# Optimization experiments

Measured on AMD Instinct MI355X. Metric: run time of the kernel, lower is better.

## Reference

```python
import jax, jax.numpy as jnp
import numpy as np

WEIGHT_HARD = 0.5
WEIGHT_SOFT = 0.5
BETA = 0.5
IGNORE_INDEX = -100
TEMPERATURE = 1.0

N_TOK = 2048
H_STU = 2048
H_TEA = 4096
VOCAB = 32000


def setup_inputs() -> dict:
    key = jax.random.key(0)
    k1, k2, k3, k4, k5 = jax.random.split(key, 5)
    scale_s = 1.0 / np.sqrt(H_STU)
    scale_t = 1.0 / np.sqrt(H_TEA)
    return {
        "student_input": jax.random.normal(k1, (N_TOK, H_STU), dtype=jnp.float32),
        "student_weight": jax.random.normal(k2, (VOCAB, H_STU), dtype=jnp.float32) * scale_s,
        "teacher_input": jax.random.normal(k3, (N_TOK, H_TEA), dtype=jnp.float32),
        "teacher_weight": jax.random.normal(k4, (VOCAB, H_TEA), dtype=jnp.float32) * scale_t,
        "true_labels": jax.random.randint(k5, (N_TOK,), 0, VOCAB, dtype=jnp.int64),
    }


def reference(student_input, student_weight, teacher_input, teacher_weight, true_labels):
    n = student_input.shape[0]
    # Fused linear projections: (BT, H) @ (H, V) -> (BT, V)
    s_logits = jnp.einsum("nh,vh->nv", student_input, student_weight).astype(jnp.float32)
    t_logits = jnp.einsum("nh,vh->nv", teacher_input, teacher_weight).astype(jnp.float32)

    # Hard loss: NLL on un-tempered student log-probs, sum over valid, / total N
    s_lp = jax.nn.log_softmax(s_logits, axis=-1)
    valid = true_labels != IGNORE_INDEX
    safe_labels = jnp.where(valid, true_labels, 0)
    picked = jnp.take_along_axis(s_lp, safe_labels[:, None], axis=1)[:, 0]
    hard_loss = jnp.sum(jnp.where(valid, -picked, 0.0)) / n

    # Soft loss: generalized JSD on temperature-scaled logits, sum over all tokens, / N
    s_lp_t = jax.nn.log_softmax(s_logits / TEMPERATURE, axis=-1)
    t_lp_t = jax.nn.log_softmax(t_logits / TEMPERATURE, axis=-1)
    s_p = jnp.exp(s_lp_t)
    t_p = jnp.exp(t_lp_t)
    log_mean = jnp.log(BETA * s_p + (1.0 - BETA) * t_p)
    student_kl = jnp.sum(s_p * (s_lp_t - log_mean))  # KL(student || mean)
    teacher_kl = jnp.sum(t_p * (t_lp_t - log_mean))  # KL(teacher || mean)
    jsd = BETA * teacher_kl + (1.0 - BETA) * student_kl
    soft_loss = jsd / n

    return WEIGHT_HARD * hard_loss + WEIGHT_SOFT * soft_loss
```

## Files before the change

kernel.cpp:

```cpp
#include <hip/hip_runtime.h>
#include <stdint.h>

#define AS1C(p) ((const __attribute__((address_space(1))) void*)(p))
#define AS3(p)  ((__attribute__((address_space(3))) void*)(p))

typedef short bf16x8 __attribute__((ext_vector_type(8)));
typedef float f32x4  __attribute__((ext_vector_type(4)));
typedef unsigned short u16x8 __attribute__((ext_vector_type(8)));

static __device__ __forceinline__ unsigned pack_bf16_2(float lo, float hi) {
  return (__float_as_uint(lo) >> 16) | (__float_as_uint(hi) & 0xFFFF0000u);
}
static __device__ __forceinline__ unsigned short bf16_rnd(float v) {
  return (unsigned short)((__float_as_uint(v) + 0x8000u) >> 16);
}
static __device__ __forceinline__ float bf16_f(unsigned short u) {
  return __uint_as_float(((unsigned)u) << 16);
}

__global__ __launch_bounds__(256) void cvt_f32_bf16(const float* __restrict__ in,
                                                    uint2* __restrict__ out,
                                                    long long n4) {
  long long i = (long long)blockIdx.x * blockDim.x + threadIdx.x;
  long long stride = (long long)gridDim.x * blockDim.x;
  const float4* in4 = (const float4*)in;
  for (; i < n4; i += stride) {
    float4 v = in4[i];
    uint2 o;
    o.x = pack_bf16_2(v.x, v.y);
    o.y = pack_bf16_2(v.z, v.w);
    out[i] = o;
  }
}


static __device__ __forceinline__ void stage2(const short* __restrict__ G, int K,
                                              int grow0, int k0,
                                              short* lds, int tid) {
  const int rl = tid >> 3;
  const int ks = ((tid & 7) ^ (rl & 7)) << 3;
  const short* src = G + (size_t)(grow0 + rl) * K + k0 + ks;
  short* dst = lds + (tid >> 6) * 512;
  __builtin_amdgcn_global_load_lds(AS1C(src), AS3(dst), 16, 0, 0);
  __builtin_amdgcn_global_load_lds(AS1C(src + (size_t)64 * K), AS3(dst + 4096), 16, 0, 0);
}

static __device__ __forceinline__ void loadB(const float* __restrict__ B, int K,
                                             int grow0, int k0, int tid, float4* r) {
  const int row = tid >> 2;
  const int kb = (tid & 3) << 4;
  const float* s = B + (size_t)(grow0 + row) * K + k0 + kb;
  r[0] = *(const float4*)(s);
  r[1] = *(const float4*)(s + 4);
  r[2] = *(const float4*)(s + 8);
  r[3] = *(const float4*)(s + 12);
}

static __device__ __forceinline__ void writeB(short* buf, int tid, const float4* r) {
  const int row = tid >> 2;
  const int g0 = (tid & 3) << 1;
  uint4 w0, w1;
  w0.x = pack_bf16_2(r[0].x, r[0].y); w0.y = pack_bf16_2(r[0].z, r[0].w);
  w0.z = pack_bf16_2(r[1].x, r[1].y); w0.w = pack_bf16_2(r[1].z, r[1].w);
  w1.x = pack_bf16_2(r[2].x, r[2].y); w1.y = pack_bf16_2(r[2].z, r[2].w);
  w1.z = pack_bf16_2(r[3].x, r[3].y); w1.w = pack_bf16_2(r[3].z, r[3].w);
  const int x = (row & 7) << 3;
  *(uint4*)(buf + row * 64 + ((g0 * 8) ^ x))       = w0;
  *(uint4*)(buf + row * 64 + (((g0 + 1) * 8) ^ x)) = w1;
}

#define MFMA16(IM0, JN0)                                                        \
  __builtin_amdgcn_s_setprio(1);                                                \
  _Pragma("unroll")                                                             \
  for (int mi = 0; mi < 4; ++mi) {                                              \
    _Pragma("unroll")                                                           \
    for (int nj = 0; nj < 2; ++nj) {                                            \
      acc[(IM0) + mi][(JN0) + nj] = __builtin_amdgcn_mfma_f32_16x16x32_bf16(    \
          a_[mi][0], b_[(JN0) + nj][0], acc[(IM0) + mi][(JN0) + nj], 0, 0, 0);  \
      acc[(IM0) + mi][(JN0) + nj] = __builtin_amdgcn_mfma_f32_16x16x32_bf16(    \
          a_[mi][1], b_[(JN0) + nj][1], acc[(IM0) + mi][(JN0) + nj], 0, 0, 0);  \
    }                                                                           \
  }                                                                             \
  __builtin_amdgcn_s_setprio(0);

__global__ __launch_bounds__(512, 2) void gemm8pf(const short* __restrict__ A,
                                                  const float* __restrict__ B,
                                                  unsigned short* __restrict__ C,
                                                  int N, int K, int mshift, int NT) {
  __shared__ __align__(16) short sA[4 * 8192];
  __shared__ __align__(16) short sB[4 * 8192];

  const int tid = threadIdx.x;
  const int lane = tid & 63;
  const int wv = tid >> 6;
  const int wm = wv >> 2;
  const int wn = wv & 3;

  const int nwg = gridDim.x;
  const int orig = blockIdx.x;
  const int q = nwg >> 3, r = nwg & 7;
  const int xcd = orig & 7;
  const int wg = (xcd < r ? xcd * (q + 1) : r * (q + 1) + (xcd - r) * q) + (orig >> 3);
  const int bm = wg & ((1 << mshift) - 1);
  const int bn = wg >> mshift;

  const int mrow0 = bm << 8;
  const int nrow0 = bn << 8;

  const int lr = lane & 15;
  const int koff0 = (((lane >> 4) << 3) ^ ((lane & 7) << 3));
  const int koff1 = ((32 + ((lane >> 4) << 3)) ^ ((lane & 7) << 3));

  f32x4 acc[8][4] = {};
  bf16x8 a_[4][2], b_[4][2];
  float4 rB0[4], rB1[4];

  stage2(A, K, mrow0,       0, sA + 0 * 8192, tid);
  stage2(A, K, mrow0 + 128, 0, sA + 1 * 8192, tid);
  loadB(B, K, nrow0,       0, tid, rB0);
  loadB(B, K, nrow0 + 128, 0, tid, rB1);
  writeB(sB + 0 * 8192, tid, rB0);
  writeB(sB + 1 * 8192, tid, rB1);
  if (NT > 1) {
    loadB(B, K, nrow0,       64, tid, rB0);
    loadB(B, K, nrow0 + 128, 64, tid, rB1);
    asm volatile("s_waitcnt vmcnt(8) lgkmcnt(0)" ::: "memory");
  } else {
    asm volatile("s_waitcnt vmcnt(0) lgkmcnt(0)" ::: "memory");
  }
  __builtin_amdgcn_s_barrier();

  for (int t = 0; t < NT; ++t) {
    const int P = t & 1;
    const short* aB = sA + (P * 2 + wm) * 8192;
    const short* bB = sB + (P * 2 + (wn >> 1)) * 8192;
    short* nxA = sA + ((P ^ 1) * 2) * 8192;
    short* nxB = sB + ((P ^ 1) * 2) * 8192;
    const int bcol = (wn & 1) * 64;

    #pragma unroll
    for (int mi = 0; mi < 4; ++mi) {
      a_[mi][0] = *(const bf16x8*)&aB[(mi * 16 + lr) * 64 + koff0];
      a_[mi][1] = *(const bf16x8*)&aB[(mi * 16 + lr) * 64 + koff1];
    }
    #pragma unroll
    for (int nj = 0; nj < 2; ++nj) {
      const int cb = (bcol + nj * 16 + lr) * 64;
      b_[nj][0] = *(const bf16x8*)&bB[cb + koff0];
      b_[nj][1] = *(const bf16x8*)&bB[cb + koff1];
    }
    if (t + 1 < NT) stage2(A, K, mrow0, (t + 1) * 64, nxA, tid);
    __builtin_amdgcn_s_barrier();
    MFMA16(0, 0)
    __builtin_amdgcn_s_barrier();

    #pragma unroll
    for (int nj = 0; nj < 2; ++nj) {
      const int cb = (bcol + (nj + 2) * 16 + lr) * 64;
      b_[nj + 2][0] = *(const bf16x8*)&bB[cb + koff0];
      b_[nj + 2][1] = *(const bf16x8*)&bB[cb + koff1];
    }
    if (t + 1 < NT) stage2(A, K, mrow0 + 128, (t + 1) * 64, nxA + 8192, tid);
    __builtin_amdgcn_s_barrier();
    MFMA16(0, 2)
    __builtin_amdgcn_s_barrier();

    #pragma unroll
    for (int mi = 0; mi < 4; ++mi) {
      a_[mi][0] = *(const bf16x8*)&aB[(64 + mi * 16 + lr) * 64 + koff0];
      a_[mi][1] = *(const bf16x8*)&aB[(64 + mi * 16 + lr) * 64 + koff1];
    }
    if (t + 1 < NT) writeB(nxB, tid, rB0);
    if (t + 2 < NT) loadB(B, K, nrow0, (t + 2) * 64, tid, rB0);
    __builtin_amdgcn_s_barrier();
    MFMA16(4, 2)
    __builtin_amdgcn_s_barrier();

    if (t + 1 < NT) writeB(nxB + 8192, tid, rB1);
    if (t + 2 < NT) loadB(B, K, nrow0 + 128, (t + 2) * 64, tid, rB1);
    __builtin_amdgcn_s_barrier();
    MFMA16(4, 0)
    if (t + 2 < NT) asm volatile("s_waitcnt vmcnt(8) lgkmcnt(0)" ::: "memory");
    else            asm volatile("s_waitcnt vmcnt(0) lgkmcnt(0)" ::: "memory");
    __builtin_amdgcn_s_barrier();
  }

  #pragma unroll
  for (int im = 0; im < 8; ++im) {
    const int row = mrow0 + wm * 128 + im * 16 + ((lane >> 4) << 2);
    #pragma unroll
    for (int ni = 0; ni < 4; ++ni) {
      const int col = nrow0 + wn * 64 + ni * 16 + lr;
      #pragma unroll
      for (int rr = 0; rr < 4; ++rr)
        C[(size_t)(row + rr) * N + col] = bf16_rnd(acc[im][ni][rr]);
    }
  }
}

__global__ __launch_bounds__(256) void gemm_lean(const float* __restrict__ A,
                                                 const float* __restrict__ B,
                                                 unsigned short* __restrict__ C,
                                                 int N, int K) {
  __shared__ __align__(16) short sA[128 * 64];
  __shared__ __align__(16) short sB[128 * 64];
  const int t = threadIdx.x;
  const int lane = t & 63;
  const int wv = t >> 6;
  const int wm = wv >> 1, wn = wv & 1;
  const int rowA0 = blockIdx.x * 128;
  const int rowB0 = blockIdx.y * 128;

  f32x4 acc[4][4] = {};

  for (int k0 = 0; k0 < K; k0 += 64) {
    #pragma unroll
    for (int i = 0; i < 8; ++i) {
      const int o = i * 1024 + t * 4;
      const int row = o >> 6;
      const int kcol = o & 63;
      const int dst = row * 64 + (kcol ^ ((row & 7) << 3));
      float4 va = *(const float4*)(A + (size_t)(rowA0 + row) * K + k0 + kcol);
      float4 vb = *(const float4*)(B + (size_t)(rowB0 + row) * K + k0 + kcol);
      uint2 pa, pb;
      pa.x = pack_bf16_2(va.x, va.y); pa.y = pack_bf16_2(va.z, va.w);
      pb.x = pack_bf16_2(vb.x, vb.y); pb.y = pack_bf16_2(vb.z, vb.w);
      *(uint2*)(sA + dst) = pa;
      *(uint2*)(sB + dst) = pb;
    }
    __syncthreads();
    #pragma unroll
    for (int kk = 0; kk < 2; ++kk) {
      bf16x8 af[4], bfr[4];
      #pragma unroll
      for (int mi = 0; mi < 4; ++mi) {
        const int row = wm * 64 + mi * 16 + (lane & 15);
        const int koff = (kk * 32 + (lane >> 4) * 8) ^ ((row & 7) << 3);
        af[mi] = *(const bf16x8*)&sA[row * 64 + koff];
      }
      #pragma unroll
      for (int ni = 0; ni < 4; ++ni) {
        const int col = wn * 64 + ni * 16 + (lane & 15);
        const int koff = (kk * 32 + (lane >> 4) * 8) ^ ((col & 7) << 3);
        bfr[ni] = *(const bf16x8*)&sB[col * 64 + koff];
      }
      #pragma unroll
      for (int mi = 0; mi < 4; ++mi)
        #pragma unroll
        for (int ni = 0; ni < 4; ++ni)
          acc[mi][ni] = __builtin_amdgcn_mfma_f32_16x16x32_bf16(af[mi], bfr[ni],
                                                                acc[mi][ni], 0, 0, 0);
    }
    __syncthreads();
  }

  #pragma unroll
  for (int mi = 0; mi < 4; ++mi)
    #pragma unroll
    for (int ni = 0; ni < 4; ++ni) {
      const int col = rowB0 + wn * 64 + ni * 16 + (lane & 15);
      const int rowb = rowA0 + wm * 64 + mi * 16 + ((lane >> 4) * 4);
      #pragma unroll
      for (int r = 0; r < 4; ++r)
        C[(size_t)(rowb + r) * N + col] = bf16_rnd(acc[mi][ni][r]);
    }
}

__global__ __launch_bounds__(512) void fused_loss(const unsigned short* __restrict__ SL,
                                                  const unsigned short* __restrict__ TL,
                                                  int V,
                                                  const int* __restrict__ labels,
                                                  int rowOff, float* __restrict__ acc) {
  __shared__ __align__(16) unsigned short bufS[32768];
  __shared__ __align__(16) unsigned short bufT[32768];
  __shared__ float red[4][8];
  const int row = blockIdx.x;
  const int tid = threadIdx.x;
  const u16x8* ps = (const u16x8*)(SL + (size_t)row * V);
  const u16x8* pt = (const u16x8*)(TL + (size_t)row * V);
  const int n8 = V >> 3;

  float ms = -1e30f, ss = 0.f, mt = -1e30f, st = 0.f;
  for (int i = tid; i < n8; i += 512) {
    u16x8 a = ps[i], b = pt[i];
    *(u16x8*)&bufS[i * 8] = a;
    *(u16x8*)&bufT[i * 8] = b;
    float lmS = -1e30f, lmT = -1e30f;
    float fa[8], fb[8];
    #pragma unroll
    for (int j = 0; j < 8; ++j) {
      fa[j] = bf16_f(a[j]); fb[j] = bf16_f(b[j]);
      lmS = fmaxf(lmS, fa[j]); lmT = fmaxf(lmT, fb[j]);
    }
    if (lmS > ms) { ss *= __expf(ms - lmS); ms = lmS; }
    if (lmT > mt) { st *= __expf(mt - lmT); mt = lmT; }
    #pragma unroll
    for (int j = 0; j < 8; ++j) {
      ss += __expf(fa[j] - ms);
      st += __expf(fb[j] - mt);
    }
  }
  #pragma unroll
  for (int off = 32; off > 0; off >>= 1) {
    float mo = __shfl_xor(ms, off), so = __shfl_xor(ss, off);
    float mn = fmaxf(ms, mo);
    ss = ss * __expf(ms - mn) + so * __expf(mo - mn); ms = mn;
    mo = __shfl_xor(mt, off); so = __shfl_xor(st, off);
    mn = fmaxf(mt, mo);
    st = st * __expf(mt - mn) + so * __expf(mo - mn); mt = mn;
  }
  const int w = tid >> 6;
  if ((tid & 63) == 0) { red[0][w] = ms; red[1][w] = ss; red[2][w] = mt; red[3][w] = st; }
  __syncthreads();
  __shared__ float lse2[2];
  if (tid == 0) {
    float M = red[0][0], S = red[1][0];
    for (int i = 1; i < 8; ++i) {
      float mn = fmaxf(M, red[0][i]);
      S = S * __expf(M - mn) + red[1][i] * __expf(red[0][i] - mn); M = mn;
    }
    lse2[0] = M + __logf(S);
    M = red[2][0]; S = red[3][0];
    for (int i = 1; i < 8; ++i) {
      float mn = fmaxf(M, red[2][i]);
      S = S * __expf(M - mn) + red[3][i] * __expf(red[2][i] - mn); M = mn;
    }
    lse2[1] = M + __logf(S);
  }
  __syncthreads();
  const float slse = lse2[0], tlse = lse2[1];
  const int lbl = labels[rowOff + row];

  float jsd = 0.f, hard = 0.f;
  for (int i = tid; i < n8; i += 512) {
    u16x8 a = *(const u16x8*)&bufS[i * 8];
    u16x8 b = *(const u16x8*)&bufT[i * 8];
    #pragma unroll
    for (int j = 0; j < 8; ++j) {
      float sl = bf16_f(a[j]) - slse;
      float tl = bf16_f(b[j]) - tlse;
      float sp = __expf(sl), tp = __expf(tl);
      float lm = __logf(0.5f * (sp + tp));
      jsd += 0.5f * (tp * (tl - lm) + sp * (sl - lm));
      if (i * 8 + j == lbl) hard = -sl;
    }
  }
  #pragma unroll
  for (int off = 32; off > 0; off >>= 1) {
    jsd += __shfl_xor(jsd, off);
    hard += __shfl_xor(hard, off);
  }
  if ((tid & 63) == 0) { red[0][w] = jsd; red[1][w] = hard; }
  __syncthreads();
  if (tid == 0) {
    float J = 0.f, H = 0.f;
    for (int i = 0; i < 8; ++i) { J += red[0][i]; H += red[1][i]; }
    atomicAdd(&acc[0], H);
    atomicAdd(&acc[1], J);
  }
}

__global__ void finalize_loss(const float* __restrict__ acc, float* __restrict__ out,
                              float invn) {
  out[0] = 0.5f * acc[0] * invn + 0.5f * acc[1] * invn;
}

extern "C" void kernel_launch(void* const* d_in, const int* in_sizes, int n_in,
                              void* d_out, int out_size, void* d_ws, size_t ws_size,
                              hipStream_t stream) {
  const float* sIn = (const float*)d_in[0];
  const float* sW  = (const float*)d_in[1];
  const float* tIn = (const float*)d_in[2];
  const float* tW  = (const float*)d_in[3];
  const int*   lbl = (const int*)d_in[4];

  const int N  = in_sizes[4];
  const int HS = in_sizes[0] / N;
  const int HT = in_sizes[2] / N;
  const int V  = in_sizes[1] / HS;

  char* ws = (char*)d_ws;
  size_t off = 0;
  auto alloc = [&](size_t b) { size_t p = off; off = (off + b + 255) & ~(size_t)255; return p; };

  const size_t o_sInB = alloc((size_t)N * HS * 2);
  const size_t o_tInB = alloc((size_t)N * HT * 2);
  const size_t o_acc  = alloc(256);

  const bool shapeOK = (V % 256 == 0) && (V <= 32768) && (V % 8 == 0) &&
                       (HS % 64 == 0) && (HT % 64 == 0) && (N % 256 == 0);
  const size_t minLogits = 2ull * 256 * V * 2 + 512;
  const bool full = shapeOK && (off + minLogits) <= ws_size;

  size_t avail = ws_size > off ? ws_size - off : 0;
  int Rfit = (int)(avail / (2ull * V * 2));
  int R = full ? 256 : 128;
  while (R * 2 <= Rfit && R * 2 <= N) R *= 2;
  const size_t o_sL = alloc((size_t)R * V * 2);
  const size_t o_tL = alloc((size_t)R * V * 2);

  hipMemsetAsync(ws + o_acc, 0, 8, stream);

  if (full) {
    auto cvt = [&](const float* src, size_t dstOff, size_t n) {
      long long n4 = (long long)(n / 4);
      int grid = (int)((n4 + 255) / 256);
      if (grid > 2048) grid = 2048;
      cvt_f32_bf16<<<grid, 256, 0, stream>>>(src, (uint2*)(ws + dstOff), n4);
    };
    cvt(sIn, o_sInB, (size_t)N * HS);
    cvt(tIn, o_tInB, (size_t)N * HT);
  }

  const int Mt = R / 256;
  int mshift = 0;
  while ((1 << mshift) < Mt) ++mshift;

  for (int r0 = 0; r0 < N; r0 += R) {
    if (full) {
      gemm8pf<<<Mt * (V / 256), 512, 0, stream>>>(
          (const short*)(ws + o_sInB + (size_t)r0 * HS * 2), sW,
          (unsigned short*)(ws + o_sL), V, HS, mshift, HS / 64);
      gemm8pf<<<Mt * (V / 256), 512, 0, stream>>>(
          (const short*)(ws + o_tInB + (size_t)r0 * HT * 2), tW,
          (unsigned short*)(ws + o_tL), V, HT, mshift, HT / 64);
    } else {
      dim3 g(R / 128, V / 128);
      gemm_lean<<<g, 256, 0, stream>>>(sIn + (size_t)r0 * HS, sW,
                                       (unsigned short*)(ws + o_sL), V, HS);
      gemm_lean<<<g, 256, 0, stream>>>(tIn + (size_t)r0 * HT, tW,
                                       (unsigned short*)(ws + o_tL), V, HT);
    }
    fused_loss<<<R, 512, 0, stream>>>((const unsigned short*)(ws + o_sL),
                                      (const unsigned short*)(ws + o_tL), V,
                                      lbl, r0, (float*)(ws + o_acc));
  }

  finalize_loss<<<1, 1, 0, stream>>>((float*)(ws + o_acc), (float*)d_out, 1.0f / N);
}
```

Measured before the change: 1.052 ms.

## Collapse GEMM inner loop to one barrier per k-tile with upfront prefetch

Restructures the main loop of the bf16 GEMM so each k-step begins by writing the next B tile and staging the next A tile into the alternate LDS buffer, then issues the B global loads two steps ahead. All B fragments are read at once and the four MFMA groups run back to back with only the final barrier kept, instead of seven barriers interleaving memory work between MFMA groups. This aims to cut barrier stalls and let the MFMA chain run uninterrupted. It also keeps more B fragments live in registers, and moves all memory issue to the start of the step, which loses the fine-grained interleave of loads with compute.

```diff
diff --git a/kernel.cpp b/kernel.cpp
--- a/kernel.cpp
+++ b/kernel.cpp
@@ -83,10 +83,10 @@
   }                                                                             \
   __builtin_amdgcn_s_setprio(0);
 
-__global__ __launch_bounds__(512, 2) void gemm8pf(const short* __restrict__ A,
-                                                  const float* __restrict__ B,
-                                                  unsigned short* __restrict__ C,
-                                                  int N, int K, int mshift, int NT) {
+__global__ __launch_bounds__(512, 2) void gemm1b(const short* __restrict__ A,
+                                                 const float* __restrict__ B,
+                                                 unsigned short* __restrict__ C,
+                                                 int N, int K, int mshift, int NT) {
   __shared__ __align__(16) short sA[4 * 8192];
   __shared__ __align__(16) short sB[4 * 8192];
 
@@ -115,10 +115,10 @@
   bf16x8 a_[4][2], b_[4][2];
   float4 rB0[4], rB1[4];
 
+  loadB(B, K, nrow0,       0, tid, rB0);
+  loadB(B, K, nrow0 + 128, 0, tid, rB1);
   stage2(A, K, mrow0,       0, sA + 0 * 8192, tid);
   stage2(A, K, mrow0 + 128, 0, sA + 1 * 8192, tid);
-  loadB(B, K, nrow0,       0, tid, rB0);
-  loadB(B, K, nrow0 + 128, 0, tid, rB1);
   writeB(sB + 0 * 8192, tid, rB0);
   writeB(sB + 1 * 8192, tid, rB1);
   if (NT > 1) {
@@ -138,48 +138,38 @@
     short* nxB = sB + ((P ^ 1) * 2) * 8192;
     const int bcol = (wn & 1) * 64;
 
+    if (t + 1 < NT) {
+      writeB(nxB,        tid, rB0);
+      writeB(nxB + 8192, tid, rB1);
+      stage2(A, K, mrow0,       (t + 1) * 64, nxA,        tid);
+      stage2(A, K, mrow0 + 128, (t + 1) * 64, nxA + 8192, tid);
+    }
+    if (t + 2 < NT) {
+      loadB(B, K, nrow0,       (t + 2) * 64, tid, rB0);
+      loadB(B, K, nrow0 + 128, (t + 2) * 64, tid, rB1);
+    }
+
+    #pragma unroll
+    for (int nj = 0; nj < 4; ++nj) {
+      const int cb = (bcol + nj * 16 + lr) * 64;
+      b_[nj][0] = *(const bf16x8*)&bB[cb + koff0];
+      b_[nj][1] = *(const bf16x8*)&bB[cb + koff1];
+    }
     #pragma unroll
     for (int mi = 0; mi < 4; ++mi) {
       a_[mi][0] = *(const bf16x8*)&aB[(mi * 16 + lr) * 64 + koff0];
       a_[mi][1] = *(const bf16x8*)&aB[(mi * 16 + lr) * 64 + koff1];
     }
-    #pragma unroll
-    for (int nj = 0; nj < 2; ++nj) {
-      const int cb = (bcol + nj * 16 + lr) * 64;
-      b_[nj][0] = *(const bf16x8*)&bB[cb + koff0];
-      b_[nj][1] = *(const bf16x8*)&bB[cb + koff1];
-    }
-    if (t + 1 < NT) stage2(A, K, mrow0, (t + 1) * 64, nxA, tid);
-    __builtin_amdgcn_s_barrier();
     MFMA16(0, 0)
-    __builtin_amdgcn_s_barrier();
-
-    #pragma unroll
-    for (int nj = 0; nj < 2; ++nj) {
-      const int cb = (bcol + (nj + 2) * 16 + lr) * 64;
-      b_[nj + 2][0] = *(const bf16x8*)&bB[cb + koff0];
-      b_[nj + 2][1] = *(const bf16x8*)&bB[cb + koff1];
-    }
-    if (t + 1 < NT) stage2(A, K, mrow0 + 128, (t + 1) * 64, nxA + 8192, tid);
-    __builtin_amdgcn_s_barrier();
     MFMA16(0, 2)
-    __builtin_amdgcn_s_barrier();
-
     #pragma unroll
     for (int mi = 0; mi < 4; ++mi) {
       a_[mi][0] = *(const bf16x8*)&aB[(64 + mi * 16 + lr) * 64 + koff0];
       a_[mi][1] = *(const bf16x8*)&aB[(64 + mi * 16 + lr) * 64 + koff1];
     }
-    if (t + 1 < NT) writeB(nxB, tid, rB0);
-    if (t + 2 < NT) loadB(B, K, nrow0, (t + 2) * 64, tid, rB0);
-    __builtin_amdgcn_s_barrier();
     MFMA16(4, 2)
-    __builtin_amdgcn_s_barrier();
-
-    if (t + 1 < NT) writeB(nxB + 8192, tid, rB1);
-    if (t + 2 < NT) loadB(B, K, nrow0 + 128, (t + 2) * 64, tid, rB1);
-    __builtin_amdgcn_s_barrier();
     MFMA16(4, 0)
+
     if (t + 2 < NT) asm volatile("s_waitcnt vmcnt(8) lgkmcnt(0)" ::: "memory");
     else            asm volatile("s_waitcnt vmcnt(0) lgkmcnt(0)" ::: "memory");
     __builtin_amdgcn_s_barrier();
@@ -418,10 +408,10 @@
 
   for (int r0 = 0; r0 < N; r0 += R) {
     if (full) {
-      gemm8pf<<<Mt * (V / 256), 512, 0, stream>>>(
+      gemm1b<<<Mt * (V / 256), 512, 0, stream>>>(
           (const short*)(ws + o_sInB + (size_t)r0 * HS * 2), sW,
           (unsigned short*)(ws + o_sL), V, HS, mshift, HS / 64);
-      gemm8pf<<<Mt * (V / 256), 512, 0, stream>>>(
+      gemm1b<<<Mt * (V / 256), 512, 0, stream>>>(
           (const short*)(ws + o_tInB + (size_t)r0 * HT * 2), tW,
           (unsigned short*)(ws + o_tL), V, HT, mshift, HT / 64);
     } else {
```

After: 1.072 ms. About the same (+1.9%).

## Merge student and teacher GEMMs and conversions into single launches; widen loss blocks

Applied to the files above, without the earlier changes.

Student and teacher projection GEMMs now run as one grid, with the first half of the blocks doing the teacher and the second half the student, so the two overlap and tail waves are shared. The two f32->bf16 conversion kernels are merged into one launch. The loss kernel moves from 512 to 1024 threads per row, with reduction arrays sized to match. This cuts launch overhead and idle tails, at the cost of uneven block durations in the merged grid and fewer resident loss blocks per CU.

```diff
diff --git a/kernel.cpp b/kernel.cpp
--- a/kernel.cpp
+++ b/kernel.cpp
@@ -18,18 +18,24 @@
   return __uint_as_float(((unsigned)u) << 16);
 }
 
-__global__ __launch_bounds__(256) void cvt_f32_bf16(const float* __restrict__ in,
-                                                    uint2* __restrict__ out,
-                                                    long long n4) {
+__global__ __launch_bounds__(256) void cvt2_f32_bf16(const float* __restrict__ inS,
+                                                     uint2* __restrict__ outS,
+                                                     long long n4s,
+                                                     const float* __restrict__ inT,
+                                                     uint2* __restrict__ outT,
+                                                     long long n4t) {
   long long i = (long long)blockIdx.x * blockDim.x + threadIdx.x;
   long long stride = (long long)gridDim.x * blockDim.x;
-  const float4* in4 = (const float4*)in;
-  for (; i < n4; i += stride) {
-    float4 v = in4[i];
+  const long long tot = n4s + n4t;
+  for (; i < tot; i += stride) {
+    const float4* src; uint2* dst; long long j;
+    if (i < n4s) { src = (const float4*)inS; dst = outS; j = i; }
+    else         { src = (const float4*)inT; dst = outT; j = i - n4s; }
+    float4 v = src[j];
     uint2 o;
     o.x = pack_bf16_2(v.x, v.y);
     o.y = pack_bf16_2(v.z, v.w);
-    out[i] = o;
+    dst[j] = o;
   }
 }
 
@@ -83,10 +89,12 @@
   }                                                                             \
   __builtin_amdgcn_s_setprio(0);
 
-__global__ __launch_bounds__(512, 2) void gemm8pf(const short* __restrict__ A,
-                                                  const float* __restrict__ B,
-                                                  unsigned short* __restrict__ C,
-                                                  int N, int K, int mshift, int NT) {
+__global__ __launch_bounds__(512, 2) void gemm_dual(
+    const short* __restrict__ A0v, const float* __restrict__ B0v,
+    unsigned short* __restrict__ C0v, int K0, int NT0,
+    const short* __restrict__ A1v, const float* __restrict__ B1v,
+    unsigned short* __restrict__ C1v, int K1, int NT1,
+    int N, int mshift, int halfGrid) {
   __shared__ __align__(16) short sA[4 * 8192];
   __shared__ __align__(16) short sB[4 * 8192];
 
@@ -96,8 +104,15 @@
   const int wm = wv >> 2;
   const int wn = wv & 3;
 
-  const int nwg = gridDim.x;
-  const int orig = blockIdx.x;
+  const bool second = (int)blockIdx.x >= halfGrid;
+  const short* A = second ? A1v : A0v;
+  const float* B = second ? B1v : B0v;
+  unsigned short* C = second ? C1v : C0v;
+  const int K  = second ? K1  : K0;
+  const int NT = second ? NT1 : NT0;
+  const int orig = (int)blockIdx.x - (second ? halfGrid : 0);
+
+  const int nwg = halfGrid;
   const int q = nwg >> 3, r = nwg & 7;
   const int xcd = orig & 7;
   const int wg = (xcd < r ? xcd * (q + 1) : r * (q + 1) + (xcd - r) * q) + (orig >> 3);
@@ -266,14 +281,14 @@
     }
 }
 
-__global__ __launch_bounds__(512) void fused_loss(const unsigned short* __restrict__ SL,
-                                                  const unsigned short* __restrict__ TL,
-                                                  int V,
-                                                  const int* __restrict__ labels,
-                                                  int rowOff, float* __restrict__ acc) {
+__global__ __launch_bounds__(1024) void fused_loss(const unsigned short* __restrict__ SL,
+                                                   const unsigned short* __restrict__ TL,
+                                                   int V,
+                                                   const int* __restrict__ labels,
+                                                   int rowOff, float* __restrict__ acc) {
   __shared__ __align__(16) unsigned short bufS[32768];
   __shared__ __align__(16) unsigned short bufT[32768];
-  __shared__ float red[4][8];
+  __shared__ float red[4][16];
   const int row = blockIdx.x;
   const int tid = threadIdx.x;
   const u16x8* ps = (const u16x8*)(SL + (size_t)row * V);
@@ -281,7 +296,7 @@
   const int n8 = V >> 3;
 
   float ms = -1e30f, ss = 0.f, mt = -1e30f, st = 0.f;
-  for (int i = tid; i < n8; i += 512) {
+  for (int i = tid; i < n8; i += 1024) {
     u16x8 a = ps[i], b = pt[i];
     *(u16x8*)&bufS[i * 8] = a;
     *(u16x8*)&bufT[i * 8] = b;
@@ -315,13 +330,13 @@
   __shared__ float lse2[2];
   if (tid == 0) {
     float M = red[0][0], S = red[1][0];
-    for (int i = 1; i < 8; ++i) {
+    for (int i = 1; i < 16; ++i) {
       float mn = fmaxf(M, red[0][i]);
       S = S * __expf(M - mn) + red[1][i] * __expf(red[0][i] - mn); M = mn;
     }
     lse2[0] = M + __logf(S);
     M = red[2][0]; S = red[3][0];
-    for (int i = 1; i < 8; ++i) {
+    for (int i = 1; i < 16; ++i) {
       float mn = fmaxf(M, red[2][i]);
       S = S * __expf(M - mn) + red[3][i] * __expf(red[2][i] - mn); M = mn;
     }
@@ -332,7 +347,7 @@
   const int lbl = labels[rowOff + row];
 
   float jsd = 0.f, hard = 0.f;
-  for (int i = tid; i < n8; i += 512) {
+  for (int i = tid; i < n8; i += 1024) {
     u16x8 a = *(const u16x8*)&bufS[i * 8];
     u16x8 b = *(const u16x8*)&bufT[i * 8];
     #pragma unroll
@@ -354,7 +369,7 @@
   __syncthreads();
   if (tid == 0) {
     float J = 0.f, H = 0.f;
-    for (int i = 0; i < 8; ++i) { J += red[0][i]; H += red[1][i]; }
+    for (int i = 0; i < 16; ++i) { J += red[0][i]; H += red[1][i]; }
     atomicAdd(&acc[0], H);
     atomicAdd(&acc[1], J);
   }
@@ -402,14 +417,12 @@
   hipMemsetAsync(ws + o_acc, 0, 8, stream);
 
   if (full) {
-    auto cvt = [&](const float* src, size_t dstOff, size_t n) {
-      long long n4 = (long long)(n / 4);
-      int grid = (int)((n4 + 255) / 256);
-      if (grid > 2048) grid = 2048;
-      cvt_f32_bf16<<<grid, 256, 0, stream>>>(src, (uint2*)(ws + dstOff), n4);
-    };
-    cvt(sIn, o_sInB, (size_t)N * HS);
-    cvt(tIn, o_tInB, (size_t)N * HT);
+    long long n4s = (long long)N * HS / 4;
+    long long n4t = (long long)N * HT / 4;
+    int grid = (int)(((n4s + n4t) + 255) / 256);
+    if (grid > 2048) grid = 2048;
+    cvt2_f32_bf16<<<grid, 256, 0, stream>>>(sIn, (uint2*)(ws + o_sInB), n4s,
+                                            tIn, (uint2*)(ws + o_tInB), n4t);
   }
 
   const int Mt = R / 256;
@@ -418,12 +431,13 @@
 
   for (int r0 = 0; r0 < N; r0 += R) {
     if (full) {
-      gemm8pf<<<Mt * (V / 256), 512, 0, stream>>>(
+      const int half = Mt * (V / 256);
+      gemm_dual<<<2 * half, 512, 0, stream>>>(
+          (const short*)(ws + o_tInB + (size_t)r0 * HT * 2), tW,
+          (unsigned short*)(ws + o_tL), HT, HT / 64,
           (const short*)(ws + o_sInB + (size_t)r0 * HS * 2), sW,
-          (unsigned short*)(ws + o_sL), V, HS, mshift, HS / 64);
-      gemm8pf<<<Mt * (V / 256), 512, 0, stream>>>(
-          (const short*)(ws + o_tInB + (size_t)r0 * HT * 2), tW,
-          (unsigned short*)(ws + o_tL), V, HT, mshift, HT / 64);
+          (unsigned short*)(ws + o_sL), HS, HS / 64,
+          V, mshift, half);
     } else {
       dim3 g(R / 128, V / 128);
       gemm_lean<<<g, 256, 0, stream>>>(sIn + (size_t)r0 * HS, sW,
@@ -431,9 +445,9 @@
       gemm_lean<<<g, 256, 0, stream>>>(tIn + (size_t)r0 * HT, tW,
                                        (unsigned short*)(ws + o_tL), V, HT);
     }
-    fused_loss<<<R, 512, 0, stream>>>((const unsigned short*)(ws + o_sL),
-                                      (const unsigned short*)(ws + o_tL), V,
-                                      lbl, r0, (float*)(ws + o_acc));
+    fused_loss<<<R, 1024, 0, stream>>>((const unsigned short*)(ws + o_sL),
+                                       (const unsigned short*)(ws + o_tL), V,
+                                       lbl, r0, (float*)(ws + o_acc));
   }
 
   finalize_loss<<<1, 1, 0, stream>>>((float*)(ws + o_acc), (float*)d_out, 1.0f / N);
```

Result: faster. 1.021 ms (median of 2 runs) (-3.0%).
